# Performance work log

Hardware: AMD Instinct MI355X
Metric: run time of the kernel (lower is better)

Reference implementation:

```python
import jax, jax.numpy as jnp
import numpy as np

B, N, D = 4, 512, 256  # batch, num_diseases, feature_dim == hidden_dim
H = 256                # hidden_dim
EPS = 1e-5

def _layernorm(x, g, b):
    m = jnp.mean(x, axis=-1, keepdims=True)
    v = jnp.mean((x - m) ** 2, axis=-1, keepdims=True)
    return (x - m) * jax.lax.rsqrt(v + EPS) * g + b

def setup_inputs() -> dict:
    key = jax.random.key(0)
    ks = jax.random.split(key, 16)
    s = 0.02
    return {
        "x": jax.random.normal(ks[0], (B, N, D), jnp.float32),
        "area_matrix": jax.random.uniform(ks[1], (B, N), jnp.float32),
        "co_occurrence": jax.random.uniform(ks[2], (N, N), jnp.float32),
        "Wq": jax.random.normal(ks[3], (H, D), jnp.float32) * s,
        "bq": jnp.zeros((H,), jnp.float32),
        "Wk": jax.random.normal(ks[4], (H, D), jnp.float32) * s,
        "bk": jnp.zeros((H,), jnp.float32),
        "Wv": jax.random.normal(ks[5], (H, D), jnp.float32) * s,
        "bv": jnp.zeros((H,), jnp.float32),
        "We1": jax.random.normal(ks[6], (H, 2), jnp.float32) * 0.5,
        "be1": jnp.zeros((H,), jnp.float32),
        "We2": jax.random.normal(ks[7], (1, H), jnp.float32) * s,
        "be2": jnp.zeros((1,), jnp.float32),
        "Wo": jax.random.normal(ks[8], (H, H), jnp.float32) * s,
        "bo": jnp.zeros((H,), jnp.float32),
        "g_ot": jnp.ones((H,), jnp.float32),
        "b_ot": jnp.zeros((H,), jnp.float32),
        "g1": jnp.ones((H,), jnp.float32),
        "b1": jnp.zeros((H,), jnp.float32),
        "g2": jnp.ones((H,), jnp.float32),
        "b2": jnp.zeros((H,), jnp.float32),
    }

def reference(x, area_matrix, co_occurrence, Wq, bq, Wk, bk, Wv, bv,
              We1, be1, We2, be2, Wo, bo, g_ot, b_ot, g1, b1, g2, b2):
    # projections: (B, N, H)
    q = jnp.einsum('bnd,hd->bnh', x, Wq) + bq
    k = jnp.einsum('bnd,hd->bnh', x, Wk) + bk
    v = jnp.einsum('bnd,hd->bnh', x, Wv) + bv
    attn_scores = jnp.einsum('bih,bjh->bij', q, k) / jnp.sqrt(jnp.float32(H))
    # edge inputs: (B, N, N, 2) = stack(broadcast area along last N, broadcast co-occ along batch)
    area = jnp.broadcast_to(area_matrix[:, :, None], (B, N, N))
    co = jnp.broadcast_to(co_occurrence[None], (B, N, N))
    edge_inputs = jnp.stack([area, co], axis=-1)
    h = jax.nn.relu(jnp.einsum('bije,he->bijh', edge_inputs, We1) + be1)
    edge_weights = jax.nn.sigmoid(jnp.einsum('bijh,oh->bijo', h, We2) + be2)[..., 0]
    attn_probs = jax.nn.softmax(attn_scores * edge_weights, axis=-1)  # dropout = identity (eval)
    out = jnp.einsum('bij,bjh->bih', attn_probs, v)
    out = _layernorm(out, g1, b1)
    out = jax.nn.relu(_layernorm(jnp.einsum('bnh,oh->bno', out, Wo) + bo, g_ot, b_ot))
    out = _layernorm(out + x, g2, b2)
    return out
```

## Files before the change

kernel.cpp:

```cpp
#include <hip/hip_runtime.h>

typedef unsigned short u16;
typedef unsigned int u32;

#define NB 4
#define NN 512
#define ND 256
#define NH 256
#define TI 4

typedef __attribute__((ext_vector_type(8))) short short8;
typedef __attribute__((ext_vector_type(4))) float f32x4;

__device__ __forceinline__ u16 f2bf(float f) {
    u32 t; __builtin_memcpy(&t, &f, 4);
    u32 r = (t + 0x7FFFu + ((t >> 16) & 1u)) >> 16;
    return (u16)r;
}

__device__ __forceinline__ float4 blockReduce4(float4 v, float4* red4b, bool ismax) {
#pragma unroll
    for (int o = 32; o > 0; o >>= 1) {
        float4 t;
        t.x = __shfl_down(v.x, o); t.y = __shfl_down(v.y, o);
        t.z = __shfl_down(v.z, o); t.w = __shfl_down(v.w, o);
        if (ismax) {
            v.x = fmaxf(v.x, t.x); v.y = fmaxf(v.y, t.y);
            v.z = fmaxf(v.z, t.z); v.w = fmaxf(v.w, t.w);
        } else {
            v.x += t.x; v.y += t.y; v.z += t.z; v.w += t.w;
        }
    }
    int wid = threadIdx.x >> 6;
    __syncthreads();
    if ((threadIdx.x & 63) == 0) red4b[wid] = v;
    __syncthreads();
    float4 r = red4b[0];
#pragma unroll
    for (int w = 1; w < 8; ++w) {
        float4 u = red4b[w];
        if (ismax) {
            r.x = fmaxf(r.x, u.x); r.y = fmaxf(r.y, u.y);
            r.z = fmaxf(r.z, u.z); r.w = fmaxf(r.w, u.w);
        } else {
            r.x += u.x; r.y += u.y; r.z += u.z; r.w += u.w;
        }
    }
    return r;
}

__global__ __launch_bounds__(256) void convert_k(
    const float* __restrict__ x, const float* __restrict__ Wq,
    const float* __restrict__ Wk, const float* __restrict__ Wv,
    u16* __restrict__ xb, u16* __restrict__ Wb)
{
    int t = blockIdx.x * 256 + threadIdx.x;
    if (t < 524288) {
        xb[t] = f2bf(x[t]);
    } else {
        int u = t - 524288;
        const float* src = (u < 65536) ? Wq : (u < 131072) ? Wk : Wv;
        Wb[u] = f2bf(src[u & 65535]);
    }
}

__global__ __launch_bounds__(256) void transpose_wo(
    const float* __restrict__ Wo, float* __restrict__ Wot)
{
    __shared__ float t[32][33];
    const int tx = threadIdx.x & 31, ty = threadIdx.x >> 5;
#pragma unroll
    for (int k = 0; k < 4; ++k)
        t[ty + 8 * k][tx] = Wo[(blockIdx.y * 32 + ty + 8 * k) * 256 + blockIdx.x * 32 + tx];
    __syncthreads();
#pragma unroll
    for (int k = 0; k < 4; ++k)
        Wot[(blockIdx.x * 32 + ty + 8 * k) * 256 + blockIdx.y * 32 + tx] = t[tx][ty + 8 * k];
}

__global__ __launch_bounds__(256) void qkv_mfma(
    const u16* __restrict__ xb, const u16* __restrict__ Wb,
    const float* __restrict__ bq, const float* __restrict__ bk, const float* __restrict__ bv,
    float* __restrict__ q, float* __restrict__ k_t, float* __restrict__ v)
{
    const int lane = threadIdx.x & 63, wave = threadIdx.x >> 6;
    const int r0 = blockIdx.x * 64 + wave * 16;
    const int out0 = blockIdx.y * 16;
    const int which = blockIdx.y >> 4;
    const float* bia = (which == 0) ? bq : (which == 1) ? bk : bv;

    const int m = lane & 15, koff = (lane >> 4) * 8;
    const u16* Ap = xb + (size_t)(r0 + m) * 256 + koff;
    const u16* Bp = Wb + (size_t)(out0 + m) * 256 + koff;

    f32x4 acc = {0.f, 0.f, 0.f, 0.f};
#pragma unroll
    for (int kb = 0; kb < 8; ++kb) {
        short8 a  = *(const short8*)(Ap + kb * 32);
        short8 bf = *(const short8*)(Bp + kb * 32);
        acc = __builtin_amdgcn_mfma_f32_16x16x32_bf16(a, bf, acc, 0, 0, 0);
    }

    const int oc = (out0 + m) & 255;
    const float bias = bia[oc];
    const int rbase = r0 + (lane >> 4) * 4;
#pragma unroll
    for (int reg = 0; reg < 4; ++reg) {
        int R = rbase + reg;
        float val = acc[reg] + bias;
        if (which == 1)      k_t[((size_t)(R >> 9) * 256 + oc) * 512 + (R & 511)] = val;
        else if (which == 0) q[(size_t)R * 256 + oc] = val;
        else                 v[(size_t)R * 256 + oc] = val;
    }
}

__global__ __launch_bounds__(512) void fused_kernel(
    const float* __restrict__ x, const float* __restrict__ area, const float* __restrict__ co,
    const float* __restrict__ We1, const float* __restrict__ be1,
    const float* __restrict__ We2, const float* __restrict__ be2,
    const float* __restrict__ Wot, const float* __restrict__ bo,
    const float* __restrict__ g_ot, const float* __restrict__ b_ot,
    const float* __restrict__ g1, const float* __restrict__ b1,
    const float* __restrict__ g2, const float* __restrict__ b2,
    const float* __restrict__ q, const float* __restrict__ k_t, const float* __restrict__ v,
    float* __restrict__ out)
{
    const int tid = threadIdx.x;
    const int b = blockIdx.x >> 7;
    const int i0 = (blockIdx.x & 127) << 2;

    __shared__ float ts[TI * 256];
    __shared__ float ea[TI * 256];
    __shared__ float eb[TI * 256];
    __shared__ float srow[TI * 512];
    __shared__ float4 red4b[8];

    const float be2f = be2[0];

    float4 bS4 = make_float4(0, 0, 0, 0), bB4 = make_float4(0, 0, 0, 0);
    if (tid < 256) {
        const float w10 = We1[2 * tid], w11 = We1[2 * tid + 1];
        const float w2v = We2[tid], be1v = be1[tid];
#pragma unroll
        for (int ti = 0; ti < TI; ++ti) {
            const float a = area[b * NN + i0 + ti];
            float al = fmaf(a, w10, be1v);
            float s = w11 * w2v, bb = al * w2v;
            float t = 3e38f, es = 0.f, ebv = 0.f, baS = 0.f, baB = 0.f;
            if (w11 == 0.f) {
                if (al > 0.f) baB = bb;
            } else {
                float tt = -al / w11;
                if (w11 > 0.f) {
                    if (tt <= 0.f)      { baS = s; baB = bb; }
                    else if (tt < 1.f)  { t = tt; es = s; ebv = bb; }
                } else {
                    if (tt >= 1.f)      { baS = s; baB = bb; }
                    else if (tt > 0.f)  { t = tt; es = -s; ebv = -bb; baS = s; baB = bb; }
                }
            }
            ts[ti * 256 + tid] = t; ea[ti * 256 + tid] = es; eb[ti * 256 + tid] = ebv;
            ((float*)&bS4)[ti] = baS; ((float*)&bB4)[ti] = baB;
        }
    }
    const float4 baseS4 = blockReduce4(bS4, red4b, false);
    const float4 baseB4 = blockReduce4(bB4, red4b, false);

    {
        const int tiS = tid >> 7, pidS = tid & 127;
        for (int k2 = 2; k2 <= 256; k2 <<= 1) {
            for (int jj = k2 >> 1; jj > 0; jj >>= 1) {
                __syncthreads();
                int low = pidS & (jj - 1);
                int t = ((pidS - low) << 1) + low;
                int p = t + jj;
                bool up = ((t & k2) == 0);
                int a0 = tiS * 256 + t, a1 = tiS * 256 + p;
                float t0 = ts[a0], t1 = ts[a1];
                if ((t0 > t1) == up) {
                    ts[a0] = t1; ts[a1] = t0;
                    float u = ea[a0]; ea[a0] = ea[a1]; ea[a1] = u;
                    u = eb[a0]; eb[a0] = eb[a1]; eb[a1] = u;
                }
            }
        }
        __syncthreads();
    }

    {
        const int colS = tid & 255, tiA = (tid >> 8) * 2;
        for (int off = 1; off < 256; off <<= 1) {
            float va0 = ea[tiA * 256 + colS],       vb0 = eb[tiA * 256 + colS];
            float va1 = ea[(tiA + 1) * 256 + colS], vb1 = eb[(tiA + 1) * 256 + colS];
            if (colS >= off) {
                va0 += ea[tiA * 256 + colS - off];       vb0 += eb[tiA * 256 + colS - off];
                va1 += ea[(tiA + 1) * 256 + colS - off]; vb1 += eb[(tiA + 1) * 256 + colS - off];
            }
            __syncthreads();
            ea[tiA * 256 + colS] = va0;       eb[tiA * 256 + colS] = vb0;
            ea[(tiA + 1) * 256 + colS] = va1; eb[(tiA + 1) * 256 + colS] = vb1;
            __syncthreads();
        }
    }

    float sA[TI];
    {
        const int j = tid;
        float dot[TI] = {0.f, 0.f, 0.f, 0.f};
        const float* kt = k_t + (size_t)b * NH * NN;
        const float* qb_ = q + (size_t)(b * NN + i0) * NH;
        for (int h = 0; h < 256; h += 4) {
            float k0 = kt[(size_t)(h + 0) * 512 + j];
            float k1 = kt[(size_t)(h + 1) * 512 + j];
            float k2c = kt[(size_t)(h + 2) * 512 + j];
            float k3 = kt[(size_t)(h + 3) * 512 + j];
#pragma unroll
            for (int ti = 0; ti < TI; ++ti) {
                float4 qv = *(const float4*)&qb_[ti * 256 + h];
                dot[ti] += qv.x * k0 + qv.y * k1 + qv.z * k2c + qv.w * k3;
            }
        }
#pragma unroll
        for (int ti = 0; ti < TI; ++ti) {
            float c = co[(size_t)(i0 + ti) * NN + j];
            int r = 0;
#pragma unroll
            for (int st = 128; st; st >>= 1)
                if (ts[ti * 256 + r + st - 1] <= c) r += st;
            float S = ((const float*)&baseS4)[ti] + (r ? ea[ti * 256 + r - 1] : 0.f);
            float B = ((const float*)&baseB4)[ti] + (r ? eb[ti * 256 + r - 1] : 0.f);
            float e = fmaf(c, S, B);
            float ew = 1.f / (1.f + __expf(-(e + be2f)));
            sA[ti] = dot[ti] * 0.0625f * ew;
        }
    }

    {
        float4 m4 = make_float4(sA[0], sA[1], sA[2], sA[3]);
        m4 = blockReduce4(m4, red4b, true);
        float eA[TI];
        float4 sum4;
#pragma unroll
        for (int ti = 0; ti < TI; ++ti) {
            eA[ti] = __expf(sA[ti] - ((const float*)&m4)[ti]);
            ((float*)&sum4)[ti] = eA[ti];
        }
        sum4 = blockReduce4(sum4, red4b, false);
#pragma unroll
        for (int ti = 0; ti < TI; ++ti)
            srow[ti * 512 + tid] = eA[ti] / ((const float*)&sum4)[ti];
        __syncthreads();
    }

    const int hP = tid & 255, half = tid >> 8;
    float accv[TI] = {0.f, 0.f, 0.f, 0.f};
    {
        const float* vp = v + (size_t)b * NN * NH + hP;
        for (int j4 = half * 64; j4 < half * 64 + 64; ++j4) {
            const int jj = 4 * j4;
            float v0 = vp[(size_t)(jj + 0) * NH];
            float v1 = vp[(size_t)(jj + 1) * NH];
            float v2 = vp[(size_t)(jj + 2) * NH];
            float v3 = vp[(size_t)(jj + 3) * NH];
#pragma unroll
            for (int ti = 0; ti < TI; ++ti) {
                float4 p4 = *(const float4*)&srow[ti * 512 + jj];
                accv[ti] += p4.x * v0 + p4.y * v1 + p4.z * v2 + p4.w * v3;
            }
        }
    }
    __syncthreads();
    if (half == 1) {
#pragma unroll
        for (int ti = 0; ti < TI; ++ti) ts[ti * 256 + hP] = accv[ti];
    }
    __syncthreads();
    if (half == 0) {
#pragma unroll
        for (int ti = 0; ti < TI; ++ti) accv[ti] += ts[ti * 256 + hP];
    }

    float4 t4;
    float dd[TI];
#pragma unroll
    for (int ti = 0; ti < TI; ++ti) ((float*)&t4)[ti] = (half == 0) ? accv[ti] : 0.f;
    float4 mean4 = blockReduce4(t4, red4b, false);
#pragma unroll
    for (int ti = 0; ti < TI; ++ti) {
        dd[ti] = (half == 0) ? accv[ti] - ((const float*)&mean4)[ti] * (1.f / 256.f) : 0.f;
        ((float*)&t4)[ti] = dd[ti] * dd[ti];
    }
    float4 var4 = blockReduce4(t4, red4b, false);
    if (half == 0) {
        const float g1v = g1[hP], b1v = b1[hP];
#pragma unroll
        for (int ti = 0; ti < TI; ++ti)
            srow[ti * 256 + hP] = dd[ti] * rsqrtf(((const float*)&var4)[ti] * (1.f / 256.f) + 1e-5f) * g1v + b1v;
    }
    __syncthreads();

    float acc2[TI] = {0.f, 0.f, 0.f, 0.f};
    {
        for (int d4 = half * 32; d4 < half * 32 + 32; ++d4) {
            const int d = 4 * d4;
            float w0 = Wot[(size_t)(d + 0) * 256 + hP];
            float w1 = Wot[(size_t)(d + 1) * 256 + hP];
            float w2c = Wot[(size_t)(d + 2) * 256 + hP];
            float w3 = Wot[(size_t)(d + 3) * 256 + hP];
#pragma unroll
            for (int ti = 0; ti < TI; ++ti) {
                float4 y4 = *(const float4*)&srow[ti * 256 + d];
                acc2[ti] += y4.x * w0 + y4.y * w1 + y4.z * w2c + y4.w * w3;
            }
        }
    }
    __syncthreads();
    if (half == 1) {
#pragma unroll
        for (int ti = 0; ti < TI; ++ti) ts[ti * 256 + hP] = acc2[ti];
    }
    __syncthreads();
    if (half == 0) {
        const float bov = bo[hP];
#pragma unroll
        for (int ti = 0; ti < TI; ++ti) acc2[ti] += ts[ti * 256 + hP] + bov;
    }

#pragma unroll
    for (int ti = 0; ti < TI; ++ti) ((float*)&t4)[ti] = (half == 0) ? acc2[ti] : 0.f;
    mean4 = blockReduce4(t4, red4b, false);
#pragma unroll
    for (int ti = 0; ti < TI; ++ti) {
        dd[ti] = (half == 0) ? acc2[ti] - ((const float*)&mean4)[ti] * (1.f / 256.f) : 0.f;
        ((float*)&t4)[ti] = dd[ti] * dd[ti];
    }
    var4 = blockReduce4(t4, red4b, false);
    float z[TI];
    const float gotv = (half == 0) ? g_ot[hP] : 0.f;
    const float botv = (half == 0) ? b_ot[hP] : 0.f;
#pragma unroll
    for (int ti = 0; ti < TI; ++ti)
        z[ti] = fmaxf(dd[ti] * rsqrtf(((const float*)&var4)[ti] * (1.f / 256.f) + 1e-5f) * gotv + botv, 0.f);

    float tt[TI];
#pragma unroll
    for (int ti = 0; ti < TI; ++ti) {
        tt[ti] = (half == 0) ? z[ti] + x[(size_t)(b * NN + i0 + ti) * ND + hP] : 0.f;
        ((float*)&t4)[ti] = tt[ti];
    }
    mean4 = blockReduce4(t4, red4b, false);
#pragma unroll
    for (int ti = 0; ti < TI; ++ti) {
        dd[ti] = (half == 0) ? tt[ti] - ((const float*)&mean4)[ti] * (1.f / 256.f) : 0.f;
        ((float*)&t4)[ti] = dd[ti] * dd[ti];
    }
    var4 = blockReduce4(t4, red4b, false);
    if (half == 0) {
        const float g2v = g2[hP], b2v = b2[hP];
#pragma unroll
        for (int ti = 0; ti < TI; ++ti) {
            float o = dd[ti] * rsqrtf(((const float*)&var4)[ti] * (1.f / 256.f) + 1e-5f) * g2v + b2v;
            out[(size_t)(b * NN + i0 + ti) * NH + hP] = o;
        }
    }
}

extern "C" void kernel_launch(void* const* d_in, const int* in_sizes, int n_in,
                              void* d_out, int out_size, void* d_ws, size_t ws_size,
                              hipStream_t stream) {
    const float* x    = (const float*)d_in[0];
    const float* area = (const float*)d_in[1];
    const float* co   = (const float*)d_in[2];
    const float* Wq   = (const float*)d_in[3];
    const float* bq   = (const float*)d_in[4];
    const float* Wk   = (const float*)d_in[5];
    const float* bk   = (const float*)d_in[6];
    const float* Wv   = (const float*)d_in[7];
    const float* bv   = (const float*)d_in[8];
    const float* We1  = (const float*)d_in[9];
    const float* be1  = (const float*)d_in[10];
    const float* We2  = (const float*)d_in[11];
    const float* be2  = (const float*)d_in[12];
    const float* Wo   = (const float*)d_in[13];
    const float* bo   = (const float*)d_in[14];
    const float* g_ot = (const float*)d_in[15];
    const float* b_ot = (const float*)d_in[16];
    const float* g1   = (const float*)d_in[17];
    const float* b1   = (const float*)d_in[18];
    const float* g2   = (const float*)d_in[19];
    const float* b2   = (const float*)d_in[20];

    float* q   = (float*)d_ws;
    float* k_t = q + (size_t)NB * NN * NH;
    float* v   = k_t + (size_t)NB * NN * NH;
    float* Wot = v + (size_t)NB * NN * NH;
    u16*   xb  = (u16*)(Wot + 256 * 256);
    u16*   Wb  = xb + (size_t)NB * NN * ND;

    convert_k<<<2816, 256, 0, stream>>>(x, Wq, Wk, Wv, xb, Wb);
    transpose_wo<<<dim3(8, 8), 256, 0, stream>>>(Wo, Wot);
    qkv_mfma<<<dim3(32, 48), 256, 0, stream>>>(xb, Wb, bq, bk, bv, q, k_t, v);
    fused_kernel<<<NB * NN / TI, 512, 0, stream>>>(x, area, co, We1, be1, We2, be2, Wot, bo,
                                                   g_ot, b_ot, g1, b1, g2, b2, q, k_t, v,
                                                   (float*)d_out);
}
```

Baseline: 175.6 us.

## Double fused kernel block to 1024 threads, replace bitonic sort with rank sort

The fused attention kernel now runs 1024 threads per block. The QK dot product, PV and Wo matmuls are split across more threads, and their partial sums are combined in shared memory. The bitonic sort of edge breakpoints is replaced by a single-pass rank-counting sort, and the scan uses ping-pong buffers with half the barriers. Each layernorm row is handled by its own waves, replacing the packed float4 block reductions. The Wo transpose is merged into the bf16 conversion kernel to save a launch. The aim is fewer serialized barrier steps and more parallelism per row tile, at the cost of more shared memory and possible register pressure with 1024 threads.

```diff
diff --git a/kernel.cpp b/kernel.cpp
--- a/kernel.cpp
+++ b/kernel.cpp
@@ -18,7 +18,13 @@
     return (u16)r;
 }
 
-__device__ __forceinline__ float4 blockReduce4(float4 v, float4* red4b, bool ismax) {
+__device__ __forceinline__ float waveReduceSum(float v) {
+#pragma unroll
+    for (int o = 32; o > 0; o >>= 1) v += __shfl_down(v, o);
+    return v;
+}
+
+__device__ __forceinline__ float4 blockReduce4w(float4 v, float4* red4, bool ismax) {
 #pragma unroll
     for (int o = 32; o > 0; o >>= 1) {
         float4 t;
@@ -33,12 +39,12 @@
     }
     int wid = threadIdx.x >> 6;
     __syncthreads();
-    if ((threadIdx.x & 63) == 0) red4b[wid] = v;
+    if ((threadIdx.x & 63) == 0) red4[wid] = v;
     __syncthreads();
-    float4 r = red4b[0];
-#pragma unroll
-    for (int w = 1; w < 8; ++w) {
-        float4 u = red4b[w];
+    float4 r = red4[0];
+#pragma unroll
+    for (int w = 1; w < 16; ++w) {
+        float4 u = red4[w];
         if (ismax) {
             r.x = fmaxf(r.x, u.x); r.y = fmaxf(r.y, u.y);
             r.z = fmaxf(r.z, u.z); r.w = fmaxf(r.w, u.w);
@@ -49,33 +55,35 @@
     return r;
 }
 
-__global__ __launch_bounds__(256) void convert_k(
+__global__ __launch_bounds__(256) void prep_kernel(
     const float* __restrict__ x, const float* __restrict__ Wq,
     const float* __restrict__ Wk, const float* __restrict__ Wv,
-    u16* __restrict__ xb, u16* __restrict__ Wb)
+    const float* __restrict__ Wo,
+    u16* __restrict__ xb, u16* __restrict__ Wb, float* __restrict__ Wot)
 {
-    int t = blockIdx.x * 256 + threadIdx.x;
-    if (t < 524288) {
-        xb[t] = f2bf(x[t]);
+    const int blk = blockIdx.x;
+    if (blk < 2816) {
+        int t = blk * 256 + threadIdx.x;
+        if (t < 524288) {
+            xb[t] = f2bf(x[t]);
+        } else {
+            int u = t - 524288;
+            const float* src = (u < 65536) ? Wq : (u < 131072) ? Wk : Wv;
+            Wb[u] = f2bf(src[u & 65535]);
+        }
     } else {
-        int u = t - 524288;
-        const float* src = (u < 65536) ? Wq : (u < 131072) ? Wk : Wv;
-        Wb[u] = f2bf(src[u & 65535]);
-    }
-}
-
-__global__ __launch_bounds__(256) void transpose_wo(
-    const float* __restrict__ Wo, float* __restrict__ Wot)
-{
-    __shared__ float t[32][33];
-    const int tx = threadIdx.x & 31, ty = threadIdx.x >> 5;
-#pragma unroll
-    for (int k = 0; k < 4; ++k)
-        t[ty + 8 * k][tx] = Wo[(blockIdx.y * 32 + ty + 8 * k) * 256 + blockIdx.x * 32 + tx];
-    __syncthreads();
-#pragma unroll
-    for (int k = 0; k < 4; ++k)
-        Wot[(blockIdx.x * 32 + ty + 8 * k) * 256 + blockIdx.y * 32 + tx] = t[tx][ty + 8 * k];
+        __shared__ float t[32][33];
+        const int t2 = blk - 2816;
+        const int bx = t2 & 7, by = t2 >> 3;
+        const int tx = threadIdx.x & 31, ty = threadIdx.x >> 5;
+#pragma unroll
+        for (int k = 0; k < 4; ++k)
+            t[ty + 8 * k][tx] = Wo[(by * 32 + ty + 8 * k) * 256 + bx * 32 + tx];
+        __syncthreads();
+#pragma unroll
+        for (int k = 0; k < 4; ++k)
+            Wot[(bx * 32 + ty + 8 * k) * 256 + by * 32 + tx] = t[tx][ty + 8 * k];
+    }
 }
 
 __global__ __launch_bounds__(256) void qkv_mfma(
@@ -114,7 +122,7 @@
     }
 }
 
-__global__ __launch_bounds__(512) void fused_kernel(
+__global__ __launch_bounds__(1024, 8) void fused_kernel(
     const float* __restrict__ x, const float* __restrict__ area, const float* __restrict__ co,
     const float* __restrict__ We1, const float* __restrict__ be1,
     const float* __restrict__ We2, const float* __restrict__ be2,
@@ -128,135 +136,143 @@
     const int tid = threadIdx.x;
     const int b = blockIdx.x >> 7;
     const int i0 = (blockIdx.x & 127) << 2;
-
-    __shared__ float ts[TI * 256];
-    __shared__ float ea[TI * 256];
-    __shared__ float eb[TI * 256];
-    __shared__ float srow[TI * 512];
-    __shared__ float4 red4b[8];
+    const int lane = tid & 63, w = tid >> 6;
+    const int tio = tid >> 8, ho = tid & 255;
+
+    __shared__ float ts[1024], ea[1024], eb[1024];
+    __shared__ float ts2[1024], ea2[1024], eb2[1024];
+    __shared__ float srow[2048];
+    __shared__ float4 red4[16];
+    __shared__ float redA[16], redB[16];
 
     const float be2f = be2[0];
 
-    float4 bS4 = make_float4(0, 0, 0, 0), bB4 = make_float4(0, 0, 0, 0);
-    if (tid < 256) {
-        const float w10 = We1[2 * tid], w11 = We1[2 * tid + 1];
-        const float w2v = We2[tid], be1v = be1[tid];
-#pragma unroll
-        for (int ti = 0; ti < TI; ++ti) {
-            const float a = area[b * NN + i0 + ti];
-            float al = fmaf(a, w10, be1v);
-            float s = w11 * w2v, bb = al * w2v;
-            float t = 3e38f, es = 0.f, ebv = 0.f, baS = 0.f, baB = 0.f;
-            if (w11 == 0.f) {
-                if (al > 0.f) baB = bb;
+    float es_v, eb_v;
+    {
+        const float w10 = We1[2 * ho], w11 = We1[2 * ho + 1];
+        const float w2v = We2[ho], be1v = be1[ho];
+        const float a = area[b * NN + i0 + tio];
+        float al = fmaf(a, w10, be1v);
+        float s = w11 * w2v, bb = al * w2v;
+        float t = 3e38f; es_v = 0.f; eb_v = 0.f;
+        float baS = 0.f, baB = 0.f;
+        if (w11 == 0.f) {
+            if (al > 0.f) baB = bb;
+        } else {
+            float tt = -al / w11;
+            if (w11 > 0.f) {
+                if (tt <= 0.f)      { baS = s; baB = bb; }
+                else if (tt < 1.f)  { t = tt; es_v = s; eb_v = bb; }
             } else {
-                float tt = -al / w11;
-                if (w11 > 0.f) {
-                    if (tt <= 0.f)      { baS = s; baB = bb; }
-                    else if (tt < 1.f)  { t = tt; es = s; ebv = bb; }
-                } else {
-                    if (tt >= 1.f)      { baS = s; baB = bb; }
-                    else if (tt > 0.f)  { t = tt; es = -s; ebv = -bb; baS = s; baB = bb; }
-                }
-            }
-            ts[ti * 256 + tid] = t; ea[ti * 256 + tid] = es; eb[ti * 256 + tid] = ebv;
-            ((float*)&bS4)[ti] = baS; ((float*)&bB4)[ti] = baB;
-        }
-    }
-    const float4 baseS4 = blockReduce4(bS4, red4b, false);
-    const float4 baseB4 = blockReduce4(bB4, red4b, false);
-
-    {
-        const int tiS = tid >> 7, pidS = tid & 127;
-        for (int k2 = 2; k2 <= 256; k2 <<= 1) {
-            for (int jj = k2 >> 1; jj > 0; jj >>= 1) {
-                __syncthreads();
-                int low = pidS & (jj - 1);
-                int t = ((pidS - low) << 1) + low;
-                int p = t + jj;
-                bool up = ((t & k2) == 0);
-                int a0 = tiS * 256 + t, a1 = tiS * 256 + p;
-                float t0 = ts[a0], t1 = ts[a1];
-                if ((t0 > t1) == up) {
-                    ts[a0] = t1; ts[a1] = t0;
-                    float u = ea[a0]; ea[a0] = ea[a1]; ea[a1] = u;
-                    u = eb[a0]; eb[a0] = eb[a1]; eb[a1] = u;
-                }
-            }
-        }
-        __syncthreads();
-    }
-
-    {
-        const int colS = tid & 255, tiA = (tid >> 8) * 2;
+                if (tt >= 1.f)      { baS = s; baB = bb; }
+                else if (tt > 0.f)  { t = tt; es_v = -s; eb_v = -bb; baS = s; baB = bb; }
+            }
+        }
+        ts[tid] = t;
+        float sS = waveReduceSum(baS);
+        float sB = waveReduceSum(baB);
+        if (lane == 0) { redA[w] = sS; redB[w] = sB; }
+        __syncthreads();
+    }
+
+    {
+        const float tm = ts[tid];
+        const float* tsb = &ts[tid & 768];
+        int cnt = 0;
+#pragma unroll 8
+        for (int hp = 0; hp < 256; ++hp) {
+            float tp = tsb[hp];
+            cnt += (tp < tm) || (tp == tm && hp < ho);
+        }
+        int dsti = (tid & 768) + cnt;
+        ts2[dsti] = tm; ea2[dsti] = es_v; eb2[dsti] = eb_v;
+        __syncthreads();
+    }
+
+    {
+        float* sa = ea2; float* sb = eb2; float* da = ea; float* db = eb;
+        const int col = ho, base = tid & 768;
         for (int off = 1; off < 256; off <<= 1) {
-            float va0 = ea[tiA * 256 + colS],       vb0 = eb[tiA * 256 + colS];
-            float va1 = ea[(tiA + 1) * 256 + colS], vb1 = eb[(tiA + 1) * 256 + colS];
-            if (colS >= off) {
-                va0 += ea[tiA * 256 + colS - off];       vb0 += eb[tiA * 256 + colS - off];
-                va1 += ea[(tiA + 1) * 256 + colS - off]; vb1 += eb[(tiA + 1) * 256 + colS - off];
-            }
+            float va = sa[base + col], vb = sb[base + col];
+            if (col >= off) { va += sa[base + col - off]; vb += sb[base + col - off]; }
+            da[base + col] = va; db[base + col] = vb;
             __syncthreads();
-            ea[tiA * 256 + colS] = va0;       eb[tiA * 256 + colS] = vb0;
-            ea[(tiA + 1) * 256 + colS] = va1; eb[(tiA + 1) * 256 + colS] = vb1;
-            __syncthreads();
-        }
-    }
-
-    float sA[TI];
-    {
-        const int j = tid;
-        float dot[TI] = {0.f, 0.f, 0.f, 0.f};
-        const float* kt = k_t + (size_t)b * NH * NN;
+            float* tmp = sa; sa = da; da = tmp;
+            tmp = sb; sb = db; db = tmp;
+        }
+    }
+
+    const int j = tid & 511, hh = tid >> 9;
+    float dotv[TI] = {0.f, 0.f, 0.f, 0.f};
+    {
+        const float* kt = k_t + (size_t)b * NH * NN + j;
         const float* qb_ = q + (size_t)(b * NN + i0) * NH;
-        for (int h = 0; h < 256; h += 4) {
-            float k0 = kt[(size_t)(h + 0) * 512 + j];
-            float k1 = kt[(size_t)(h + 1) * 512 + j];
-            float k2c = kt[(size_t)(h + 2) * 512 + j];
-            float k3 = kt[(size_t)(h + 3) * 512 + j];
+        for (int h = hh * 128; h < hh * 128 + 128; h += 4) {
+            float k0 = kt[(size_t)(h + 0) * 512];
+            float k1 = kt[(size_t)(h + 1) * 512];
+            float k2c = kt[(size_t)(h + 2) * 512];
+            float k3 = kt[(size_t)(h + 3) * 512];
 #pragma unroll
             for (int ti = 0; ti < TI; ++ti) {
                 float4 qv = *(const float4*)&qb_[ti * 256 + h];
-                dot[ti] += qv.x * k0 + qv.y * k1 + qv.z * k2c + qv.w * k3;
-            }
-        }
+                dotv[ti] += qv.x * k0 + qv.y * k1 + qv.z * k2c + qv.w * k3;
+            }
+        }
+        if (hh == 1) {
+#pragma unroll
+            for (int ti = 0; ti < TI; ++ti) srow[ti * 512 + j] = dotv[ti];
+        }
+        __syncthreads();
+        if (hh == 0) {
+#pragma unroll
+            for (int ti = 0; ti < TI; ++ti) dotv[ti] += srow[ti * 512 + j];
+        }
+    }
+
+    {
+        float sA[TI] = {-3e38f, -3e38f, -3e38f, -3e38f};
+        if (hh == 0) {
+#pragma unroll
+            for (int ti = 0; ti < TI; ++ti) {
+                float c = co[(size_t)(i0 + ti) * NN + j];
+                int r = 0;
+                const float* tz = &ts2[ti * 256];
+#pragma unroll
+                for (int st = 128; st; st >>= 1)
+                    if (tz[r + st - 1] <= c) r += st;
+                float bS = redA[ti * 4] + redA[ti * 4 + 1] + redA[ti * 4 + 2] + redA[ti * 4 + 3];
+                float bB = redB[ti * 4] + redB[ti * 4 + 1] + redB[ti * 4 + 2] + redB[ti * 4 + 3];
+                float S = bS + (r ? ea2[ti * 256 + r - 1] : 0.f);
+                float B = bB + (r ? eb2[ti * 256 + r - 1] : 0.f);
+                float e = fmaf(c, S, B) + be2f;
+                float ew = 1.f / (1.f + __expf(-e));
+                sA[ti] = dotv[ti] * 0.0625f * ew;
+            }
+        }
+        float4 m4 = make_float4(sA[0], sA[1], sA[2], sA[3]);
+        m4 = blockReduce4w(m4, red4, true);
+        float eA[TI];
+        float4 s4;
 #pragma unroll
         for (int ti = 0; ti < TI; ++ti) {
-            float c = co[(size_t)(i0 + ti) * NN + j];
-            int r = 0;
-#pragma unroll
-            for (int st = 128; st; st >>= 1)
-                if (ts[ti * 256 + r + st - 1] <= c) r += st;
-            float S = ((const float*)&baseS4)[ti] + (r ? ea[ti * 256 + r - 1] : 0.f);
-            float B = ((const float*)&baseB4)[ti] + (r ? eb[ti * 256 + r - 1] : 0.f);
-            float e = fmaf(c, S, B);
-            float ew = 1.f / (1.f + __expf(-(e + be2f)));
-            sA[ti] = dot[ti] * 0.0625f * ew;
-        }
-    }
-
-    {
-        float4 m4 = make_float4(sA[0], sA[1], sA[2], sA[3]);
-        m4 = blockReduce4(m4, red4b, true);
-        float eA[TI];
-        float4 sum4;
-#pragma unroll
-        for (int ti = 0; ti < TI; ++ti) {
-            eA[ti] = __expf(sA[ti] - ((const float*)&m4)[ti]);
-            ((float*)&sum4)[ti] = eA[ti];
-        }
-        sum4 = blockReduce4(sum4, red4b, false);
-#pragma unroll
-        for (int ti = 0; ti < TI; ++ti)
-            srow[ti * 512 + tid] = eA[ti] / ((const float*)&sum4)[ti];
-        __syncthreads();
-    }
-
-    const int hP = tid & 255, half = tid >> 8;
-    float accv[TI] = {0.f, 0.f, 0.f, 0.f};
-    {
-        const float* vp = v + (size_t)b * NN * NH + hP;
-        for (int j4 = half * 64; j4 < half * 64 + 64; ++j4) {
+            eA[ti] = (hh == 0) ? __expf(sA[ti] - ((const float*)&m4)[ti]) : 0.f;
+            ((float*)&s4)[ti] = eA[ti];
+        }
+        s4 = blockReduce4w(s4, red4, false);
+        if (hh == 0) {
+#pragma unroll
+            for (int ti = 0; ti < TI; ++ti)
+                srow[ti * 512 + j] = eA[ti] * (1.f / ((const float*)&s4)[ti]);
+        }
+        __syncthreads();
+    }
+
+    float acc1;
+    {
+        const int qtr = tid >> 8;
+        float accv[TI] = {0.f, 0.f, 0.f, 0.f};
+        const float* vp = v + (size_t)b * NN * NH + ho;
+        for (int j4 = qtr * 32; j4 < qtr * 32 + 32; ++j4) {
             const int jj = 4 * j4;
             float v0 = vp[(size_t)(jj + 0) * NH];
             float v1 = vp[(size_t)(jj + 1) * NH];
@@ -268,100 +284,77 @@
                 accv[ti] += p4.x * v0 + p4.y * v1 + p4.z * v2 + p4.w * v3;
             }
         }
-    }
-    __syncthreads();
-    if (half == 1) {
-#pragma unroll
-        for (int ti = 0; ti < TI; ++ti) ts[ti * 256 + hP] = accv[ti];
-    }
-    __syncthreads();
-    if (half == 0) {
-#pragma unroll
-        for (int ti = 0; ti < TI; ++ti) accv[ti] += ts[ti * 256 + hP];
-    }
-
-    float4 t4;
-    float dd[TI];
-#pragma unroll
-    for (int ti = 0; ti < TI; ++ti) ((float*)&t4)[ti] = (half == 0) ? accv[ti] : 0.f;
-    float4 mean4 = blockReduce4(t4, red4b, false);
-#pragma unroll
-    for (int ti = 0; ti < TI; ++ti) {
-        dd[ti] = (half == 0) ? accv[ti] - ((const float*)&mean4)[ti] * (1.f / 256.f) : 0.f;
-        ((float*)&t4)[ti] = dd[ti] * dd[ti];
-    }
-    float4 var4 = blockReduce4(t4, red4b, false);
-    if (half == 0) {
-        const float g1v = g1[hP], b1v = b1[hP];
-#pragma unroll
-        for (int ti = 0; ti < TI; ++ti)
-            srow[ti * 256 + hP] = dd[ti] * rsqrtf(((const float*)&var4)[ti] * (1.f / 256.f) + 1e-5f) * g1v + b1v;
-    }
-    __syncthreads();
-
-    float acc2[TI] = {0.f, 0.f, 0.f, 0.f};
-    {
-        for (int d4 = half * 32; d4 < half * 32 + 32; ++d4) {
+        float* pq = (qtr == 0) ? ts2 : (qtr == 1) ? ts : (qtr == 2) ? ea : eb;
+#pragma unroll
+        for (int ti = 0; ti < TI; ++ti) pq[ti * 256 + ho] = accv[ti];
+        __syncthreads();
+        acc1 = ts2[tid] + ts[tid] + ea[tid] + eb[tid];
+    }
+
+    {
+        float s = waveReduceSum(acc1);
+        if (lane == 0) redA[w] = s;
+        __syncthreads();
+        float mean = (redA[tio * 4] + redA[tio * 4 + 1] + redA[tio * 4 + 2] + redA[tio * 4 + 3]) * (1.f / 256.f);
+        float dd = acc1 - mean;
+        float s2 = waveReduceSum(dd * dd);
+        if (lane == 0) redB[w] = s2;
+        __syncthreads();
+        float var = (redB[tio * 4] + redB[tio * 4 + 1] + redB[tio * 4 + 2] + redB[tio * 4 + 3]) * (1.f / 256.f);
+        srow[tid] = dd * rsqrtf(var + 1e-5f) * g1[ho] + b1[ho];
+        __syncthreads();
+    }
+
+    float acc2o;
+    {
+        const int qtr = tid >> 8;
+        float acc2[TI] = {0.f, 0.f, 0.f, 0.f};
+        for (int d4 = qtr * 16; d4 < qtr * 16 + 16; ++d4) {
             const int d = 4 * d4;
-            float w0 = Wot[(size_t)(d + 0) * 256 + hP];
-            float w1 = Wot[(size_t)(d + 1) * 256 + hP];
-            float w2c = Wot[(size_t)(d + 2) * 256 + hP];
-            float w3 = Wot[(size_t)(d + 3) * 256 + hP];
+            float w0 = Wot[(size_t)(d + 0) * 256 + ho];
+            float w1 = Wot[(size_t)(d + 1) * 256 + ho];
+            float w2c = Wot[(size_t)(d + 2) * 256 + ho];
+            float w3 = Wot[(size_t)(d + 3) * 256 + ho];
 #pragma unroll
             for (int ti = 0; ti < TI; ++ti) {
                 float4 y4 = *(const float4*)&srow[ti * 256 + d];
                 acc2[ti] += y4.x * w0 + y4.y * w1 + y4.z * w2c + y4.w * w3;
             }
         }
-    }
-    __syncthreads();
-    if (half == 1) {
-#pragma unroll
-        for (int ti = 0; ti < TI; ++ti) ts[ti * 256 + hP] = acc2[ti];
-    }
-    __syncthreads();
-    if (half == 0) {
-        const float bov = bo[hP];
-#pragma unroll
-        for (int ti = 0; ti < TI; ++ti) acc2[ti] += ts[ti * 256 + hP] + bov;
-    }
-
-#pragma unroll
-    for (int ti = 0; ti < TI; ++ti) ((float*)&t4)[ti] = (half == 0) ? acc2[ti] : 0.f;
-    mean4 = blockReduce4(t4, red4b, false);
-#pragma unroll
-    for (int ti = 0; ti < TI; ++ti) {
-        dd[ti] = (half == 0) ? acc2[ti] - ((const float*)&mean4)[ti] * (1.f / 256.f) : 0.f;
-        ((float*)&t4)[ti] = dd[ti] * dd[ti];
-    }
-    var4 = blockReduce4(t4, red4b, false);
-    float z[TI];
-    const float gotv = (half == 0) ? g_ot[hP] : 0.f;
-    const float botv = (half == 0) ? b_ot[hP] : 0.f;
-#pragma unroll
-    for (int ti = 0; ti < TI; ++ti)
-        z[ti] = fmaxf(dd[ti] * rsqrtf(((const float*)&var4)[ti] * (1.f / 256.f) + 1e-5f) * gotv + botv, 0.f);
-
-    float tt[TI];
-#pragma unroll
-    for (int ti = 0; ti < TI; ++ti) {
-        tt[ti] = (half == 0) ? z[ti] + x[(size_t)(b * NN + i0 + ti) * ND + hP] : 0.f;
-        ((float*)&t4)[ti] = tt[ti];
-    }
-    mean4 = blockReduce4(t4, red4b, false);
-#pragma unroll
-    for (int ti = 0; ti < TI; ++ti) {
-        dd[ti] = (half == 0) ? tt[ti] - ((const float*)&mean4)[ti] * (1.f / 256.f) : 0.f;
-        ((float*)&t4)[ti] = dd[ti] * dd[ti];
-    }
-    var4 = blockReduce4(t4, red4b, false);
-    if (half == 0) {
-        const float g2v = g2[hP], b2v = b2[hP];
-#pragma unroll
-        for (int ti = 0; ti < TI; ++ti) {
-            float o = dd[ti] * rsqrtf(((const float*)&var4)[ti] * (1.f / 256.f) + 1e-5f) * g2v + b2v;
-            out[(size_t)(b * NN + i0 + ti) * NH + hP] = o;
-        }
+        float* pq = (qtr == 0) ? ts2 : (qtr == 1) ? ts : (qtr == 2) ? ea : eb;
+#pragma unroll
+        for (int ti = 0; ti < TI; ++ti) pq[ti * 256 + ho] = acc2[ti];
+        __syncthreads();
+        acc2o = ts2[tid] + ts[tid] + ea[tid] + eb[tid] + bo[ho];
+    }
+
+    float z;
+    {
+        float s = waveReduceSum(acc2o);
+        if (lane == 0) redA[w] = s;
+        __syncthreads();
+        float mean = (redA[tio * 4] + redA[tio * 4 + 1] + redA[tio * 4 + 2] + redA[tio * 4 + 3]) * (1.f / 256.f);
+        float dd = acc2o - mean;
+        float s2 = waveReduceSum(dd * dd);
+        if (lane == 0) redB[w] = s2;
+        __syncthreads();
+        float var = (redB[tio * 4] + redB[tio * 4 + 1] + redB[tio * 4 + 2] + redB[tio * 4 + 3]) * (1.f / 256.f);
+        z = fmaxf(dd * rsqrtf(var + 1e-5f) * g_ot[ho] + b_ot[ho], 0.f);
+    }
+
+    {
+        float tt = z + x[(size_t)(b * NN + i0 + tio) * ND + ho];
+        float s = waveReduceSum(tt);
+        if (lane == 0) redA[w] = s;
+        __syncthreads();
+        float mean = (redA[tio * 4] + redA[tio * 4 + 1] + redA[tio * 4 + 2] + redA[tio * 4 + 3]) * (1.f / 256.f);
+        float dd = tt - mean;
+        float s2 = waveReduceSum(dd * dd);
+        if (lane == 0) redB[w] = s2;
+        __syncthreads();
+        float var = (redB[tio * 4] + redB[tio * 4 + 1] + redB[tio * 4 + 2] + redB[tio * 4 + 3]) * (1.f / 256.f);
+        float o = dd * rsqrtf(var + 1e-5f) * g2[ho] + b2[ho];
+        out[(size_t)(b * NN + i0 + tio) * NH + ho] = o;
     }
 }
 
@@ -397,10 +390,9 @@
     u16*   xb  = (u16*)(Wot + 256 * 256);
     u16*   Wb  = xb + (size_t)NB * NN * ND;
 
-    convert_k<<<2816, 256, 0, stream>>>(x, Wq, Wk, Wv, xb, Wb);
-    transpose_wo<<<dim3(8, 8), 256, 0, stream>>>(Wo, Wot);
+    prep_kernel<<<2880, 256, 0, stream>>>(x, Wq, Wk, Wv, Wo, xb, Wb, Wot);
     qkv_mfma<<<dim3(32, 48), 256, 0, stream>>>(xb, Wb, bq, bk, bv, q, k_t, v);
-    fused_kernel<<<NB * NN / TI, 512, 0, stream>>>(x, area, co, We1, be1, We2, be2, Wot, bo,
-                                                   g_ot, b_ot, g1, b1, g2, b2, q, k_t, v,
-                                                   (float*)d_out);
-}
+    fused_kernel<<<NB * NN / TI, 1024, 0, stream>>>(x, area, co, We1, be1, We2, be2, Wot, bo,
+                                                    g_ot, b_ot, g1, b1, g2, b2, q, k_t, v,
+                                                    (float*)d_out);
+}
```

After: 192.2 us. 1.09x slower.
